# Kernel optimization log

Measured on AMD Instinct MI355X. Metric: run time of the kernel, lower is better.

## Reference

```python
import jax, jax.numpy as jnp
import numpy as np

B, S, L = 8, 64, 6          # graphs, spatial side, orientation layers
K = 6                       # Chebyshev order
IN_D, HID, OUT_D = 3, 128, 10


def _grid_edges(num_graphs, s, l):
    b, o, y, x = np.meshgrid(np.arange(num_graphs), np.arange(l), np.arange(s), np.arange(s), indexing='ij')
    nid = ((b * l + o) * s + y) * s + x  # linear node id, [B,L,s,s]
    srcs, dsts = [], []
    def add(a, c):
        srcs.append(a.ravel()); dsts.append(c.ravel())
    add(nid[..., :-1], nid[..., 1:]); add(nid[..., 1:], nid[..., :-1])                 # x-neighbors
    add(nid[:, :, :-1, :], nid[:, :, 1:, :]); add(nid[:, :, 1:, :], nid[:, :, :-1, :])  # y-neighbors
    nxt = np.roll(nid, -1, axis=1)                                                     # orientation ring
    add(nid, nxt); add(nxt, nid)
    return np.stack([np.concatenate(srcs), np.concatenate(dsts)]).astype(np.int32)


def _cluster_spatial(num_graphs, s, l):
    b, o, y, x = np.meshgrid(np.arange(num_graphs), np.arange(l), np.arange(s), np.arange(s), indexing='ij')
    h = s // 2
    return (((b * l + o) * h + y // 2) * h + x // 2).ravel().astype(np.int32)


def setup_inputs() -> dict:
    key = jax.random.key(0)
    ks = jax.random.split(key, 20)
    inp = {}
    N1 = B * L * S * S
    inp['x'] = jax.random.normal(ks[0], (N1, IN_D), jnp.float32)
    for i, s in enumerate([S, S // 2, S // 4]):
        ei = _grid_edges(B, s, L)
        inp[f'edge_index{i+1}'] = jnp.asarray(ei)
        inp[f'edge_attr{i+1}'] = jax.random.uniform(ks[1 + i], (ei.shape[1],), jnp.float32, 0.1, 1.0)
    inp['cluster1'] = jnp.asarray(_cluster_spatial(B, S, L))
    inp['cluster2'] = jnp.asarray(_cluster_spatial(B, S // 2, L))
    inp['cluster3'] = jnp.asarray(_cluster_spatial(B, S // 4, L))
    s4 = S // 8
    b, o, y, x = np.meshgrid(np.arange(B), np.arange(L), np.arange(s4), np.arange(s4), indexing='ij')
    inp['cluster4'] = jnp.asarray(((b * s4 + y) * s4 + x).ravel().astype(np.int32))  # collapse orientation axis
    inp['batch_final'] = jnp.asarray(np.repeat(np.arange(B), s4 * s4).astype(np.int32))
    dims = [(IN_D, HID), (HID, HID), (HID, HID), (HID, HID), (HID, HID), (HID, OUT_D)]
    for i, (di, do) in enumerate(dims):
        inp[f'W{i+1}'] = jax.random.normal(ks[8 + i], (K, di, do), jnp.float32) / np.float32(np.sqrt(di * K))
        inp[f'b{i+1}'] = jnp.zeros((do,), jnp.float32)
    for i in range(5):
        inp[f'gamma{i+1}'] = jnp.ones((HID,), jnp.float32)
        inp[f'beta{i+1}'] = jnp.zeros((HID,), jnp.float32)
    return inp


def _cheb_conv(x, ei, ea, W, b):
    # Chebyshev polynomial graph conv: out = sum_k T_k(L) x @ W_k + b,
    # with T0=x, T1=Lx, Tk = 2 L T_{k-1} - T_{k-2}; L applied via edge gather/scatter.
    src, dst = ei[0], ei[1]
    n = x.shape[0]
    def lap(v):
        return jax.ops.segment_sum(ea[:, None] * v[src], dst, num_segments=n)
    Tx0 = x
    out = Tx0 @ W[0]
    Tx1 = lap(x)
    out = out + Tx1 @ W[1]
    for k in range(2, W.shape[0]):
        Tx2 = 2.0 * lap(Tx1) - Tx0
        out = out + Tx2 @ W[k]
        Tx0, Tx1 = Tx1, Tx2
    return out + b


def _bn(x, g, bt):
    # BatchNorm1d in training mode (batch statistics, biased variance, eps=1e-5)
    mu = x.mean(0)
    var = x.var(0)
    return g * (x - mu) * jax.lax.rsqrt(var + 1e-5) + bt


def reference(x, edge_index1, edge_attr1, edge_index2, edge_attr2, edge_index3, edge_attr3, cluster1, cluster2, cluster3, cluster4, batch_final, W1, b1, W2, b2, W3, b3, W4, b4, W5, b5, W6, b6, gamma1, beta1, gamma2, beta2, gamma3, beta3, gamma4, beta4, gamma5, beta5):
    h = jax.nn.relu(_bn(_cheb_conv(x, edge_index1, edge_attr1, W1, b1), gamma1, beta1))
    h = jax.nn.relu(_bn(_cheb_conv(h, edge_index1, edge_attr1, W2, b2), gamma2, beta2))
    h = jax.ops.segment_max(h, cluster1, num_segments=B * L * (S // 2) ** 2)
    h = jax.nn.relu(_bn(_cheb_conv(h, edge_index2, edge_attr2, W3, b3), gamma3, beta3))
    h = jax.nn.relu(_bn(_cheb_conv(h, edge_index2, edge_attr2, W4, b4), gamma4, beta4))
    h = jax.ops.segment_max(h, cluster2, num_segments=B * L * (S // 4) ** 2)
    h = jax.nn.relu(_bn(_cheb_conv(h, edge_index3, edge_attr3, W5, b5), gamma5, beta5))
    h = jax.nn.relu(_cheb_conv(h, edge_index3, edge_attr3, W6, b6))
    h = jax.ops.segment_max(h, cluster3, num_segments=B * L * (S // 8) ** 2)   # spatial pool 3
    h = jax.ops.segment_max(h, cluster4, num_segments=B * (S // 8) ** 2)        # orientation pool
    g = jax.ops.segment_max(h, batch_final, num_segments=B)                     # global max pool
    return jax.nn.log_softmax(g, axis=1)
```

## Files before the change

kernel.cpp:

```cpp
#include <hip/hip_runtime.h>
#include <math.h>

#define L_OR 6
#define N_BL 48

typedef unsigned short u16;
typedef __attribute__((ext_vector_type(8))) short s8v;
typedef __attribute__((ext_vector_type(4))) float f4v;

#define N1 196608
#define N2 49152
#define N3 12288
#define LSTRIDE 114688

__device__ u16   g_cat[(size_t)N1 * 768 + 1024];
__device__ u16   g_O[(size_t)N1 * 128];
__device__ float g_Tt[5 * (size_t)N1 * 3];
__device__ u16   g_Bt[4 * LSTRIDE];
__device__ u16   g_W6t[16 * 768];
__device__ float g_wt1[(size_t)N1 * 8];
__device__ float g_wt2[(size_t)N2 * 8];
__device__ float g_wt3[(size_t)N3 * 8];
__device__ float g_O10[(size_t)N3 * 10];
__device__ float g_part[1536 * 256];
__device__ float g_part2[64 * 256];
__device__ float g_gsc[128];
__device__ float g_gso[128];
__device__ unsigned g_cnt;

__device__ __forceinline__ float b2f(u16 v) {
    return __uint_as_float(((unsigned)v) << 16);
}
__device__ __forceinline__ u16 f2b(float f) {
    unsigned u = __float_as_uint(f);
    return (u16)((u + 0x7FFFu + ((u >> 16) & 1u)) >> 16);
}

__global__ __launch_bounds__(256)
void eaprep_all(float* __restrict__ wt1, float* __restrict__ wt2,
                float* __restrict__ wt3, const float* __restrict__ ea1,
                const float* __restrict__ ea2, const float* __restrict__ ea3)
{
    int idx = blockIdx.x * 256 + threadIdx.x;
    int S, n; float* wtab; const float* ea;
    if (idx < N1)            { S = 64; wtab = wt1; ea = ea1; n = idx; }
    else if (idx < N1 + N2)  { S = 32; wtab = wt2; ea = ea2; n = idx - N1; }
    else if (idx < N1 + N2 + N3) { S = 16; wtab = wt3; ea = ea3; n = idx - N1 - N2; }
    else return;
    int x = n % S, y = (n / S) % S, g = n / (S * S);
    int o = g % L_OR, b = g / L_OR;
    const int szx = N_BL * S * (S - 1);
    const int basex = (g * S + y) * (S - 1);
    float wxm = (x > 0)     ? ea[basex + x - 1] : 0.f;
    float wxp = (x < S - 1) ? ea[szx + basex + x] : 0.f;
    float wym = (y > 0)     ? ea[2 * szx + (g * (S - 1) + y - 1) * S + x] : 0.f;
    float wyp = (y < S - 1) ? ea[3 * szx + (g * (S - 1) + y) * S + x] : 0.f;
    int op_ = (o == 0) ? L_OR - 1 : o - 1;
    int on_ = (o == L_OR - 1) ? 0 : o + 1;
    int sp = ((b * L_OR + op_) * S + y) * S + x;
    int sn = ((b * L_OR + on_) * S + y) * S + x;
    float wom = ea[4 * szx + sp];
    float wop = ea[4 * szx + N_BL * S * S + n];
    float* w = wtab + (size_t)n * 8;
    w[0] = wxm; w[1] = wxp; w[2] = wym; w[3] = wyp; w[4] = wom; w[5] = wop;
    ((int*)w)[6] = sp - n;
    ((int*)w)[7] = sn - n;
}

template<int S>
__global__ __launch_bounds__(256)
void lap128b(u16* __restrict__ cat, int outSlot, int inSlot, int tppSlot,
             const float* __restrict__ wtab, float alpha)
{
    const int NN = N_BL * S * S;
    int node = blockIdx.x * 16 + (threadIdx.x >> 4);
    int c8   = threadIdx.x & 15;

    float4 wa = *(const float4*)(wtab + (size_t)node * 8);
    float4 wb = *(const float4*)(wtab + (size_t)node * 8 + 4);
    int dsp = __float_as_int(wb.z);
    int dsn = __float_as_int(wb.w);
    int sxm = (node > 0)      ? node - 1 : 0;
    int sxp = (node < NN - 1) ? node + 1 : node;
    int sym = (node >= S)     ? node - S : node;
    int syp = (node < NN - S) ? node + S : node;

    const int chOff = inSlot * 128 + c8 * 8;
    float a[8] = {0.f, 0.f, 0.f, 0.f, 0.f, 0.f, 0.f, 0.f};
    auto gather = [&](int src, float w) {
        s8v v = *(const s8v*)(cat + (size_t)src * 768 + chOff);
#pragma unroll
        for (int j = 0; j < 8; ++j) a[j] += w * b2f((u16)v[j]);
    };
    gather(sxm, wa.x); gather(sxp, wa.y); gather(sym, wa.z); gather(syp, wa.w);
    gather(node + dsp, wb.x); gather(node + dsn, wb.y);

    float r[8];
#pragma unroll
    for (int j = 0; j < 8; ++j) r[j] = alpha * a[j];
    if (tppSlot >= 0) {
        s8v t = *(const s8v*)(cat + (size_t)node * 768 + tppSlot * 128 + c8 * 8);
#pragma unroll
        for (int j = 0; j < 8; ++j) r[j] -= b2f((u16)t[j]);
    }
    uint4 ov;
    asm("v_cvt_pk_bf16_f32 %0, %1, %2" : "=v"(ov.x) : "v"(r[0]), "v"(r[1]));
    asm("v_cvt_pk_bf16_f32 %0, %1, %2" : "=v"(ov.y) : "v"(r[2]), "v"(r[3]));
    asm("v_cvt_pk_bf16_f32 %0, %1, %2" : "=v"(ov.z) : "v"(r[4]), "v"(r[5]));
    asm("v_cvt_pk_bf16_f32 %0, %1, %2" : "=v"(ov.w) : "v"(r[6]), "v"(r[7]));
    *(uint4*)(cat + (size_t)node * 768 + outSlot * 128 + c8 * 8) = ov;
}

template<int S>
__global__ __launch_bounds__(256)
void lap1bn(u16* __restrict__ cat, const u16* __restrict__ O,
            int t0Slot, int t1Slot, const float* __restrict__ wtab,
            const float* __restrict__ gsc, const float* __restrict__ gso)
{
    const int NN = N_BL * S * S;
    int node = blockIdx.x * 16 + (threadIdx.x >> 4);
    int c8   = threadIdx.x & 15;

    float4 wa = *(const float4*)(wtab + (size_t)node * 8);
    float4 wb = *(const float4*)(wtab + (size_t)node * 8 + 4);
    int dsp = __float_as_int(wb.z);
    int dsn = __float_as_int(wb.w);
    int sxm = (node > 0)      ? node - 1 : 0;
    int sxp = (node < NN - 1) ? node + 1 : node;
    int sym = (node >= S)     ? node - S : node;
    int syp = (node < NN - S) ? node + S : node;

    float sc[8], so[8];
    {
        float4 s0 = *(const float4*)(gsc + c8 * 8);
        float4 s1 = *(const float4*)(gsc + c8 * 8 + 4);
        float4 o0 = *(const float4*)(gso + c8 * 8);
        float4 o1 = *(const float4*)(gso + c8 * 8 + 4);
        sc[0]=s0.x; sc[1]=s0.y; sc[2]=s0.z; sc[3]=s0.w;
        sc[4]=s1.x; sc[5]=s1.y; sc[6]=s1.z; sc[7]=s1.w;
        so[0]=o0.x; so[1]=o0.y; so[2]=o0.z; so[3]=o0.w;
        so[4]=o1.x; so[5]=o1.y; so[6]=o1.z; so[7]=o1.w;
    }

    float a[8] = {0.f, 0.f, 0.f, 0.f, 0.f, 0.f, 0.f, 0.f};
    auto gatherbn = [&](int src, float w) {
        s8v v = *(const s8v*)(O + (size_t)src * 128 + c8 * 8);
#pragma unroll
        for (int j = 0; j < 8; ++j)
            a[j] += w * fmaxf(b2f((u16)v[j]) * sc[j] + so[j], 0.f);
    };
    gatherbn(sxm, wa.x); gatherbn(sxp, wa.y); gatherbn(sym, wa.z); gatherbn(syp, wa.w);
    gatherbn(node + dsp, wb.x); gatherbn(node + dsn, wb.y);

    float t0[8];
    {
        s8v v = *(const s8v*)(O + (size_t)node * 128 + c8 * 8);
#pragma unroll
        for (int j = 0; j < 8; ++j)
            t0[j] = fmaxf(b2f((u16)v[j]) * sc[j] + so[j], 0.f);
    }
    uint4 o0v, o1v;
    asm("v_cvt_pk_bf16_f32 %0, %1, %2" : "=v"(o0v.x) : "v"(t0[0]), "v"(t0[1]));
    asm("v_cvt_pk_bf16_f32 %0, %1, %2" : "=v"(o0v.y) : "v"(t0[2]), "v"(t0[3]));
    asm("v_cvt_pk_bf16_f32 %0, %1, %2" : "=v"(o0v.z) : "v"(t0[4]), "v"(t0[5]));
    asm("v_cvt_pk_bf16_f32 %0, %1, %2" : "=v"(o0v.w) : "v"(t0[6]), "v"(t0[7]));
    asm("v_cvt_pk_bf16_f32 %0, %1, %2" : "=v"(o1v.x) : "v"(a[0]), "v"(a[1]));
    asm("v_cvt_pk_bf16_f32 %0, %1, %2" : "=v"(o1v.y) : "v"(a[2]), "v"(a[3]));
    asm("v_cvt_pk_bf16_f32 %0, %1, %2" : "=v"(o1v.z) : "v"(a[4]), "v"(a[5]));
    asm("v_cvt_pk_bf16_f32 %0, %1, %2" : "=v"(o1v.w) : "v"(a[6]), "v"(a[7]));
    *(uint4*)(cat + (size_t)node * 768 + t0Slot * 128 + c8 * 8) = o0v;
    *(uint4*)(cat + (size_t)node * 768 + t1Slot * 128 + c8 * 8) = o1v;
}

template<int S>
__global__ __launch_bounds__(256)
void lap3_kernel(float* __restrict__ out, const float* __restrict__ in,
                 const float* __restrict__ tpp, const float* __restrict__ wtab,
                 float alpha)
{
    const int NN = N_BL * S * S;
    int n = blockIdx.x * 256 + threadIdx.x;
    if (n >= NN) return;
    float4 wa = *(const float4*)(wtab + (size_t)n * 8);
    float4 wb = *(const float4*)(wtab + (size_t)n * 8 + 4);
    int dsp = __float_as_int(wb.z);
    int dsn = __float_as_int(wb.w);
    int sxm = (n > 0)      ? n - 1 : 0;
    int sxp = (n < NN - 1) ? n + 1 : n;
    int sym = (n >= S)     ? n - S : n;
    int syp = (n < NN - S) ? n + S : n;

    float a0 = 0.f, a1 = 0.f, a2 = 0.f;
    auto gather = [&](int src, float w) {
        a0 += w * in[src * 3 + 0];
        a1 += w * in[src * 3 + 1];
        a2 += w * in[src * 3 + 2];
    };
    gather(sxm, wa.x); gather(sxp, wa.y); gather(sym, wa.z); gather(syp, wa.w);
    gather(n + dsp, wb.x); gather(n + dsn, wb.y);

    float r0 = alpha * a0, r1 = alpha * a1, r2 = alpha * a2;
    if (tpp) { r0 -= tpp[n * 3 + 0]; r1 -= tpp[n * 3 + 1]; r2 -= tpp[n * 3 + 2]; }
    out[n * 3 + 0] = r0; out[n * 3 + 1] = r1; out[n * 3 + 2] = r2;
}

__global__ __launch_bounds__(256)
void gemm_mfma_cat(u16* __restrict__ O, const u16* __restrict__ A,
                   const u16* __restrict__ Bf, const float* __restrict__ bias,
                   float* __restrict__ partials)
{
    __shared__ u16 Bs[4][4096];
    const int tid  = threadIdx.x;
    const int wave = tid >> 6;
    const int lane = tid & 63;
    const int lrow = lane & 15;
    const int kg   = lane >> 4;
    const int r0   = blockIdx.x * 128 + wave * 32;

    const u16* A0 = A + (size_t)(r0 + lrow) * 768 + kg * 8;
    const u16* A1 = A0 + (size_t)16 * 768;

    f4v acc[2][8] = {};

#pragma unroll
    for (int i = 0; i < 4; ++i) {
        *(s8v*)&Bs[i][tid * 8]        = *(const s8v*)(Bf + i * 4096 + tid * 8);
        *(s8v*)&Bs[i][2048 + tid * 8] = *(const s8v*)(Bf + i * 4096 + 2048 + tid * 8);
    }
    s8v a0 = *(const s8v*)(A0);
    s8v a1 = *(const s8v*)(A1);
    __syncthreads();

#pragma unroll 1
    for (int p = 0; p < 24; ++p) {
        const int pl = (p + 4 < 24) ? p + 4 : 23;
        s8v nb0 = *(const s8v*)(Bf + pl * 4096 + tid * 8);
        s8v nb1 = *(const s8v*)(Bf + pl * 4096 + 2048 + tid * 8);
        s8v na0 = *(const s8v*)(A0 + (p + 1) * 32);
        s8v na1 = *(const s8v*)(A1 + (p + 1) * 32);
        const u16* bsl = &Bs[p & 3][0];
#pragma unroll
        for (int ct = 0; ct < 8; ++ct) {
            s8v b = *(const s8v*)&bsl[(ct * 64 + lane) * 8];
            acc[0][ct] = __builtin_amdgcn_mfma_f32_16x16x32_bf16(a0, b, acc[0][ct], 0, 0, 0);
            acc[1][ct] = __builtin_amdgcn_mfma_f32_16x16x32_bf16(a1, b, acc[1][ct], 0, 0, 0);
        }
        __syncthreads();
        *(s8v*)&Bs[p & 3][tid * 8]        = nb0;
        *(s8v*)&Bs[p & 3][2048 + tid * 8] = nb1;
        a0 = na0; a1 = na1;
    }

    __shared__ float sred[4][2][8][16];
    float cs[8], cq[8];
#pragma unroll
    for (int ct = 0; ct < 8; ++ct) { cs[ct] = 0.f; cq[ct] = 0.f; }

#pragma unroll
    for (int s = 0; s < 2; ++s)
#pragma unroll
        for (int ct = 0; ct < 8; ++ct) {
            int col = ct * 16 + lrow;
            float bv = bias[col];
#pragma unroll
            for (int j = 0; j < 4; ++j) {
                int row = r0 + s * 16 + kg * 4 + j;
                float v = acc[s][ct][j] + bv;
                O[(size_t)row * 128 + col] = f2b(v);
                cs[ct] += v; cq[ct] += v * v;
            }
        }
#pragma unroll
    for (int ct = 0; ct < 8; ++ct) {
        cs[ct] += __shfl_xor(cs[ct], 16); cs[ct] += __shfl_xor(cs[ct], 32);
        cq[ct] += __shfl_xor(cq[ct], 16); cq[ct] += __shfl_xor(cq[ct], 32);
    }
    __syncthreads();
    if (lane < 16) {
#pragma unroll
        for (int ct = 0; ct < 8; ++ct) {
            sred[wave][0][ct][lane] = cs[ct];
            sred[wave][1][ct][lane] = cq[ct];
        }
    }
    __syncthreads();
    if (threadIdx.x < 128) {
        int ct = threadIdx.x >> 4, lr = threadIdx.x & 15;
        float S = 0.f, Q = 0.f;
#pragma unroll
        for (int w = 0; w < 4; ++w) { S += sred[w][0][ct][lr]; Q += sred[w][1][ct][lr]; }
        partials[blockIdx.x * 256 + threadIdx.x]       = S;
        partials[blockIdx.x * 256 + 128 + threadIdx.x] = Q;
    }
}

__global__ __launch_bounds__(256)
void wprep_all(const float* __restrict__ W2, const float* __restrict__ W3,
               const float* __restrict__ W4, const float* __restrict__ W5,
               u16* __restrict__ Bf)
{
    int l = blockIdx.y;
    const float* W = (l == 0) ? W2 : (l == 1) ? W3 : (l == 2) ? W4 : W5;
    int base = (l & 1) ? 5 : 0;
    int idx = blockIdx.x * 256 + threadIdx.x;
    int j    = idx & 7;
    int lane = (idx >> 3) & 63;
    int ct   = (idx >> 9) & 7;
    int k0s  = idx >> 12;
    int k    = k0s * 32 + (lane >> 4) * 8 + j;
    int col  = ct * 16 + (lane & 15);
    int slot = k >> 7, d = k & 127;
    int wk = slot - base; if (wk < 0) wk += 6;
    Bf[(size_t)l * LSTRIDE + idx] = f2b(W[(size_t)wk * 16384 + d * 128 + col]);
}

__global__ __launch_bounds__(256)
void w6prep(const float* __restrict__ W, u16* __restrict__ W6t, int base)
{
    int idx = blockIdx.x * 256 + threadIdx.x;
    if (idx >= 16 * 768) return;
    int c = idx / 768, kk = idx % 768;
    int slot = kk >> 7, d = kk & 127;
    int wk = slot - base; if (wk < 0) wk += 6;
    W6t[idx] = (c < 10) ? f2b(W[(size_t)wk * 1280 + d * 10 + c]) : (u16)0;
}

__global__ __launch_bounds__(256)
void l1gemm(u16* __restrict__ O, const float* __restrict__ T0,
            const float* __restrict__ Tt, const float* __restrict__ W,
            const float* __restrict__ bias, float* __restrict__ partials)
{
    __shared__ float Ts[128][18];
    __shared__ float sh[2][128], sh2[2][128];
    int tid = threadIdx.x;
    int rbase = blockIdx.x * 128;
    for (int i = tid; i < 128 * 18; i += 256) {
        int r = i / 18, t = i % 18;
        int k = t / 3, j = t % 3;
        Ts[r][t] = (k == 0) ? T0[(size_t)(rbase + r) * 3 + j]
                            : Tt[(size_t)(k - 1) * N1 * 3 + (size_t)(rbase + r) * 3 + j];
    }
    __syncthreads();
    int c = tid & 127, h = tid >> 7;
    float w[18];
#pragma unroll
    for (int k = 0; k < 6; ++k)
#pragma unroll
        for (int j = 0; j < 3; ++j) w[k * 3 + j] = W[(size_t)k * 384 + j * 128 + c];
    float bv = bias[c];
    float S = 0.f, Q = 0.f;
    for (int i = 0; i < 64; ++i) {
        int r = h * 64 + i;
        float acc = bv;
#pragma unroll
        for (int t = 0; t < 18; ++t) acc += Ts[r][t] * w[t];
        O[(size_t)(rbase + r) * 128 + c] = f2b(acc);
        S += acc; Q += acc * acc;
    }
    sh[h][c] = S; sh2[h][c] = Q;
    __syncthreads();
    if (tid < 128) {
        partials[blockIdx.x * 256 + tid]       = sh[0][tid] + sh[1][tid];
        partials[blockIdx.x * 256 + 128 + tid] = sh2[0][tid] + sh2[1][tid];
    }
}

__global__ __launch_bounds__(256)
void out10_cat(float* __restrict__ O10, const u16* __restrict__ cat,
               const u16* __restrict__ W6t, const float* __restrict__ bias)
{
    int col = threadIdx.x & 15;
    int row = blockIdx.x * 16 + (threadIdx.x >> 4);
    const u16* a = cat + (size_t)row * 768;
    const u16* w = W6t + (size_t)col * 768;
    float acc = 0.f;
#pragma unroll 4
    for (int k0 = 0; k0 < 768; k0 += 8) {
        s8v av = *(const s8v*)(a + k0);
        s8v wv = *(const s8v*)(w + k0);
#pragma unroll
        for (int j = 0; j < 8; ++j)
            acc += b2f((u16)av[j]) * b2f((u16)wv[j]);
    }
    if (col < 10)
        O10[(size_t)row * 10 + col] = fmaxf(acc + bias[col], 0.f);
}

__global__ __launch_bounds__(256)
void bn_reduce_f(const float* __restrict__ partials, int nblk, int N,
                 const float* __restrict__ g, const float* __restrict__ bt,
                 float* __restrict__ gsc, float* __restrict__ gso,
                 float* __restrict__ part2, unsigned* __restrict__ cnt)
{
    int tid = threadIdx.x;
    float S = 0.f;
#pragma unroll 4
    for (int b = blockIdx.x; b < nblk; b += 64)
        S += partials[(size_t)b * 256 + tid];
    part2[blockIdx.x * 256 + tid] = S;
    __threadfence();
    __syncthreads();
    __shared__ int last;
    if (tid == 0) last = (atomicAdd(cnt, 1u) == 63u) ? 1 : 0;
    __syncthreads();
    if (!last) return;
    __threadfence();
    int c = tid & 127, h = tid >> 7;
    float Sa = 0.f, Qa = 0.f;
#pragma unroll 8
    for (int b = h; b < 64; b += 2) {
        Sa += part2[b * 256 + c];
        Qa += part2[b * 256 + 128 + c];
    }
    __shared__ float shS[2][128], shQ[2][128];
    shS[h][c] = Sa; shQ[h][c] = Qa;
    __syncthreads();
    if (tid < 128) {
        float Sx = shS[0][tid] + shS[1][tid];
        float Qx = shQ[0][tid] + shQ[1][tid];
        float inv_n = 1.f / (float)N;
        float mu = Sx * inv_n;
        float var = Qx * inv_n - mu * mu;
        float is = rsqrtf(var + 1e-5f);
        float sc = is * g[tid];
        gsc[tid] = sc;
        gso[tid] = bt[tid] - mu * sc;
    }
    if (tid == 0) *cnt = 0u;
}

__global__ __launch_bounds__(256)
void bn_apply_pool8(const u16* __restrict__ O, u16* __restrict__ cat, int outSlot,
                    int s, int Nout,
                    const float* __restrict__ gsc, const float* __restrict__ gso)
{
    int idx = blockIdx.x * 256 + threadIdx.x;
    if (idx >= Nout * 16) return;
    int c8 = idx & 15;
    int n2 = idx >> 4;
    int h  = s >> 1;
    int x2 = n2 % h;
    int y2 = (n2 / h) % h;
    int gg = n2 / (h * h);
    int base = (gg * s + 2 * y2) * s + 2 * x2;
    s8v v0 = *(const s8v*)(O + (size_t)base * 128 + c8 * 8);
    s8v v1 = *(const s8v*)(O + (size_t)(base + 1) * 128 + c8 * 8);
    s8v v2 = *(const s8v*)(O + (size_t)(base + s) * 128 + c8 * 8);
    s8v v3 = *(const s8v*)(O + (size_t)(base + s + 1) * 128 + c8 * 8);
    s8v ov;
#pragma unroll
    for (int j = 0; j < 8; ++j) {
        int c = c8 * 8 + j;
        float sc = gsc[c], so = gso[c];
        float m =          b2f((u16)v0[j]) * sc + so;
        m = fmaxf(m, b2f((u16)v1[j]) * sc + so);
        m = fmaxf(m, b2f((u16)v2[j]) * sc + so);
        m = fmaxf(m, b2f((u16)v3[j]) * sc + so);
        ov[j] = (short)f2b(fmaxf(m, 0.f));
    }
    *(s8v*)(cat + (size_t)n2 * 768 + outSlot * 128 + c8 * 8) = ov;
}

__global__ __launch_bounds__(512)
void tail_fused(const float* __restrict__ O10, float* __restrict__ out)
{
    __shared__ float p4[512][10];
    __shared__ float G[8][10];
    __shared__ float rowm[8], rowl[8];
    int t = threadIdx.x;
    for (int i = t; i < 5120; i += 512) {
        int c = i % 10, n = i / 10;
        int x = n & 7, y = (n >> 3) & 7, b = n >> 6;
        float m = -INFINITY;
        for (int o = 0; o < L_OR; ++o) {
            int base = ((b * L_OR + o) * 16 + 2 * y) * 16 + 2 * x;
            m = fmaxf(m, O10[(size_t)base * 10 + c]);
            m = fmaxf(m, O10[(size_t)(base + 1) * 10 + c]);
            m = fmaxf(m, O10[(size_t)(base + 16) * 10 + c]);
            m = fmaxf(m, O10[(size_t)(base + 17) * 10 + c]);
        }
        p4[n][c] = m;
    }
    __syncthreads();
    if (t < 80) {
        int b = t / 10, c = t % 10;
        float m = -INFINITY;
        for (int p = 0; p < 64; ++p) m = fmaxf(m, p4[b * 64 + p][c]);
        G[b][c] = m;
    }
    __syncthreads();
    if (t < 8) {
        float m = -INFINITY;
        for (int c = 0; c < 10; ++c) m = fmaxf(m, G[t][c]);
        float s = 0.f;
        for (int c = 0; c < 10; ++c) s += expf(G[t][c] - m);
        rowm[t] = m; rowl[t] = logf(s);
    }
    __syncthreads();
    if (t < 80) {
        int b = t / 10, c = t % 10;
        out[t] = G[b][c] - rowm[b] - rowl[b];
    }
}

static void launch_lapb(u16* cat, int os, int is, int ts, const float* wtab,
                        int S, int N, float alpha, hipStream_t st)
{
    dim3 grid(N / 16), block(256);
    if (S == 64)      hipLaunchKernelGGL(lap128b<64>, grid, block, 0, st, cat, os, is, ts, wtab, alpha);
    else if (S == 32) hipLaunchKernelGGL(lap128b<32>, grid, block, 0, st, cat, os, is, ts, wtab, alpha);
    else              hipLaunchKernelGGL(lap128b<16>, grid, block, 0, st, cat, os, is, ts, wtab, alpha);
}

static void cheb_laps_b5(u16* cat, const float* wtab, int S, int N, hipStream_t st)
{
    for (int k = 1; k < 6; ++k) {
        int os = (k + 5) % 6;
        int is = (k - 1 + 5) % 6;
        int ts = (k >= 2) ? (k - 2 + 5) % 6 : -1;
        launch_lapb(cat, os, is, ts, wtab, S, N, (k == 1) ? 1.f : 2.f, st);
    }
}

static void cheb_laps_2to5(u16* cat, const float* wtab, int S, int N, hipStream_t st)
{
    for (int k = 2; k < 6; ++k)
        launch_lapb(cat, k, k - 1, k - 2, wtab, S, N, 2.f, st);
}

static void launch_lap1bn(u16* cat, const u16* O, const float* wtab,
                          const float* gsc, const float* gso,
                          int S, int N, hipStream_t st)
{
    dim3 grid(N / 16), block(256);
    if (S == 64)      hipLaunchKernelGGL(lap1bn<64>, grid, block, 0, st, cat, O, 0, 1, wtab, gsc, gso);
    else if (S == 32) hipLaunchKernelGGL(lap1bn<32>, grid, block, 0, st, cat, O, 0, 1, wtab, gsc, gso);
    else              hipLaunchKernelGGL(lap1bn<16>, grid, block, 0, st, cat, O, 0, 1, wtab, gsc, gso);
}

extern "C" void kernel_launch(void* const* d_in, const int* in_sizes, int n_in,
                              void* d_out, int out_size, void* d_ws, size_t ws_size,
                              hipStream_t stream)
{
    const float* x   = (const float*)d_in[0];
    const float* ea1 = (const float*)d_in[2];
    const float* ea2 = (const float*)d_in[4];
    const float* ea3 = (const float*)d_in[6];
    const float* W1  = (const float*)d_in[12];
    const float* b1  = (const float*)d_in[13];
    const float* W2  = (const float*)d_in[14];
    const float* b2  = (const float*)d_in[15];
    const float* W3  = (const float*)d_in[16];
    const float* b3  = (const float*)d_in[17];
    const float* W4  = (const float*)d_in[18];
    const float* b4  = (const float*)d_in[19];
    const float* W5  = (const float*)d_in[20];
    const float* b5  = (const float*)d_in[21];
    const float* W6  = (const float*)d_in[22];
    const float* b6  = (const float*)d_in[23];
    const float* g1  = (const float*)d_in[24];
    const float* be1 = (const float*)d_in[25];
    const float* g2  = (const float*)d_in[26];
    const float* be2 = (const float*)d_in[27];
    const float* g3  = (const float*)d_in[28];
    const float* be3 = (const float*)d_in[29];
    const float* g4  = (const float*)d_in[30];
    const float* be4 = (const float*)d_in[31];
    const float* g5  = (const float*)d_in[32];
    const float* be5 = (const float*)d_in[33];

    u16 *cat, *O, *Bt, *W6t;
    float *Tt, *O10, *part, *part2, *gsc, *gso, *wt1, *wt2, *wt3;
    unsigned* cnt;
    if (hipGetSymbolAddress((void**)&cat, HIP_SYMBOL(g_cat)) != hipSuccess) return;
    if (hipGetSymbolAddress((void**)&O,   HIP_SYMBOL(g_O))   != hipSuccess) return;
    if (hipGetSymbolAddress((void**)&Tt,  HIP_SYMBOL(g_Tt))  != hipSuccess) return;
    if (hipGetSymbolAddress((void**)&Bt,  HIP_SYMBOL(g_Bt))  != hipSuccess) return;
    if (hipGetSymbolAddress((void**)&W6t, HIP_SYMBOL(g_W6t)) != hipSuccess) return;
    if (hipGetSymbolAddress((void**)&O10, HIP_SYMBOL(g_O10)) != hipSuccess) return;
    if (hipGetSymbolAddress((void**)&part,  HIP_SYMBOL(g_part))  != hipSuccess) return;
    if (hipGetSymbolAddress((void**)&part2, HIP_SYMBOL(g_part2)) != hipSuccess) return;
    if (hipGetSymbolAddress((void**)&gsc, HIP_SYMBOL(g_gsc)) != hipSuccess) return;
    if (hipGetSymbolAddress((void**)&gso, HIP_SYMBOL(g_gso)) != hipSuccess) return;
    if (hipGetSymbolAddress((void**)&wt1, HIP_SYMBOL(g_wt1)) != hipSuccess) return;
    if (hipGetSymbolAddress((void**)&wt2, HIP_SYMBOL(g_wt2)) != hipSuccess) return;
    if (hipGetSymbolAddress((void**)&wt3, HIP_SYMBOL(g_wt3)) != hipSuccess) return;
    if (hipGetSymbolAddress((void**)&cnt, HIP_SYMBOL(g_cnt)) != hipSuccess) return;

    dim3 blk(256);

    hipLaunchKernelGGL(eaprep_all, dim3((N1 + N2 + N3) / 256), blk, 0, stream,
                       wt1, wt2, wt3, ea1, ea2, ea3);
    hipLaunchKernelGGL(wprep_all, dim3(384, 4), blk, 0, stream, W2, W3, W4, W5, Bt);
    hipLaunchKernelGGL(w6prep, dim3(48), blk, 0, stream, W6, W6t, 0);

    {
        float* t1 = Tt;
        float* t2 = Tt + (size_t)N1 * 3;
        float* t3 = Tt + (size_t)2 * N1 * 3;
        float* t4 = Tt + (size_t)3 * N1 * 3;
        float* t5 = Tt + (size_t)4 * N1 * 3;
        dim3 gl((N1 + 255) / 256);
        hipLaunchKernelGGL(lap3_kernel<64>, gl, blk, 0, stream, t1, x,  (const float*)nullptr, wt1, 1.f);
        hipLaunchKernelGGL(lap3_kernel<64>, gl, blk, 0, stream, t2, t1, x,  wt1, 2.f);
        hipLaunchKernelGGL(lap3_kernel<64>, gl, blk, 0, stream, t3, t2, t1, wt1, 2.f);
        hipLaunchKernelGGL(lap3_kernel<64>, gl, blk, 0, stream, t4, t3, t2, wt1, 2.f);
        hipLaunchKernelGGL(lap3_kernel<64>, gl, blk, 0, stream, t5, t4, t3, wt1, 2.f);
        hipLaunchKernelGGL(l1gemm, dim3(N1 / 128), blk, 0, stream, O, x, Tt, W1, b1, part);
    }
    hipLaunchKernelGGL(bn_reduce_f, dim3(64), blk, 0, stream, part, N1 / 128, N1,
                       g1, be1, gsc, gso, part2, cnt);

    launch_lap1bn(cat, O, wt1, gsc, gso, 64, N1, stream);
    cheb_laps_2to5(cat, wt1, 64, N1, stream);
    hipLaunchKernelGGL(gemm_mfma_cat, dim3(N1 / 128), blk, 0, stream, O, cat, Bt, b2, part);
    hipLaunchKernelGGL(bn_reduce_f, dim3(64), blk, 0, stream, part, N1 / 128, N1,
                       g2, be2, gsc, gso, part2, cnt);
    hipLaunchKernelGGL(bn_apply_pool8, dim3(N2 / 16), blk, 0, stream,
                       O, cat, 5, 64, N2, gsc, gso);

    cheb_laps_b5(cat, wt2, 32, N2, stream);
    hipLaunchKernelGGL(gemm_mfma_cat, dim3(N2 / 128), blk, 0, stream, O, cat, Bt + 1 * LSTRIDE, b3, part);
    hipLaunchKernelGGL(bn_reduce_f, dim3(64), blk, 0, stream, part, N2 / 128, N2,
                       g3, be3, gsc, gso, part2, cnt);

    launch_lap1bn(cat, O, wt2, gsc, gso, 32, N2, stream);
    cheb_laps_2to5(cat, wt2, 32, N2, stream);
    hipLaunchKernelGGL(gemm_mfma_cat, dim3(N2 / 128), blk, 0, stream, O, cat, Bt + 2 * LSTRIDE, b4, part);
    hipLaunchKernelGGL(bn_reduce_f, dim3(64), blk, 0, stream, part, N2 / 128, N2,
                       g4, be4, gsc, gso, part2, cnt);
    hipLaunchKernelGGL(bn_apply_pool8, dim3(N3 / 16), blk, 0, stream,
                       O, cat, 5, 32, N3, gsc, gso);

    cheb_laps_b5(cat, wt3, 16, N3, stream);
    hipLaunchKernelGGL(gemm_mfma_cat, dim3(N3 / 128), blk, 0, stream, O, cat, Bt + 3 * LSTRIDE, b5, part);
    hipLaunchKernelGGL(bn_reduce_f, dim3(64), blk, 0, stream, part, N3 / 128, N3,
                       g5, be5, gsc, gso, part2, cnt);

    launch_lap1bn(cat, O, wt3, gsc, gso, 16, N3, stream);
    cheb_laps_2to5(cat, wt3, 16, N3, stream);
    hipLaunchKernelGGL(out10_cat, dim3(N3 / 16), blk, 0, stream, O10, cat, W6t, b6);

    hipLaunchKernelGGL(tail_fused, dim3(1), dim3(512), 0, stream, O10, (float*)d_out);
}
```

Before: 787.7 us.

## Stage GEMM weights via direct global-to-LDS loads with double buffering

The MFMA GEMM now copies each weight tile straight from global memory into LDS with global_load_lds, instead of loading into registers and then storing to shared memory. It double-buffers 64-wide K chunks (12 iterations instead of 24), which halves the number of barriers and drops one redundant sync in the epilogue. The W6 prep kernel is folded into wprep_all as a fifth grid row, saving a launch. The risk is the prefetch distance: it shrinks from four chunks to one, so global latency may be less well hidden.

```diff
diff --git a/kernel.cpp b/kernel.cpp
--- a/kernel.cpp
+++ b/kernel.cpp
@@ -209,7 +209,7 @@
                    const u16* __restrict__ Bf, const float* __restrict__ bias,
                    float* __restrict__ partials)
 {
-    __shared__ u16 Bs[4][4096];
+    __shared__ u16 Bs[2][8192];
     const int tid  = threadIdx.x;
     const int wave = tid >> 6;
     const int lane = tid & 63;
@@ -222,33 +222,46 @@
 
     f4v acc[2][8] = {};
 
-#pragma unroll
-    for (int i = 0; i < 4; ++i) {
-        *(s8v*)&Bs[i][tid * 8]        = *(const s8v*)(Bf + i * 4096 + tid * 8);
-        *(s8v*)&Bs[i][2048 + tid * 8] = *(const s8v*)(Bf + i * 4096 + 2048 + tid * 8);
-    }
-    s8v a0 = *(const s8v*)(A0);
-    s8v a1 = *(const s8v*)(A1);
+    auto stage = [&](int q, int slot) {
+        const char* src = (const char*)(Bf + q * 8192) + wave * 4096 + lane * 16;
+        char* dstb = (char*)(&Bs[slot][0]) + wave * 4096;
+#pragma unroll
+        for (int i = 0; i < 4; ++i)
+            __builtin_amdgcn_global_load_lds(
+                (const __attribute__((address_space(1))) unsigned*)(src + i * 1024),
+                (__attribute__((address_space(3))) unsigned*)(dstb + i * 1024),
+                16, 0, 0);
+    };
+
+    stage(0, 0);
+    s8v a00 = *(const s8v*)(A0);
+    s8v a10 = *(const s8v*)(A1);
+    s8v a01 = *(const s8v*)(A0 + 32);
+    s8v a11 = *(const s8v*)(A1 + 32);
     __syncthreads();
 
 #pragma unroll 1
-    for (int p = 0; p < 24; ++p) {
-        const int pl = (p + 4 < 24) ? p + 4 : 23;
-        s8v nb0 = *(const s8v*)(Bf + pl * 4096 + tid * 8);
-        s8v nb1 = *(const s8v*)(Bf + pl * 4096 + 2048 + tid * 8);
-        s8v na0 = *(const s8v*)(A0 + (p + 1) * 32);
-        s8v na1 = *(const s8v*)(A1 + (p + 1) * 32);
-        const u16* bsl = &Bs[p & 3][0];
+    for (int p = 0; p < 12; ++p) {
+        stage(p + 1, (p + 1) & 1);
+        s8v na00 = *(const s8v*)(A0 + (p + 1) * 64);
+        s8v na10 = *(const s8v*)(A1 + (p + 1) * 64);
+        s8v na01 = *(const s8v*)(A0 + (p + 1) * 64 + 32);
+        s8v na11 = *(const s8v*)(A1 + (p + 1) * 64 + 32);
+        const u16* bsl = &Bs[p & 1][0];
 #pragma unroll
         for (int ct = 0; ct < 8; ++ct) {
             s8v b = *(const s8v*)&bsl[(ct * 64 + lane) * 8];
-            acc[0][ct] = __builtin_amdgcn_mfma_f32_16x16x32_bf16(a0, b, acc[0][ct], 0, 0, 0);
-            acc[1][ct] = __builtin_amdgcn_mfma_f32_16x16x32_bf16(a1, b, acc[1][ct], 0, 0, 0);
+            acc[0][ct] = __builtin_amdgcn_mfma_f32_16x16x32_bf16(a00, b, acc[0][ct], 0, 0, 0);
+            acc[1][ct] = __builtin_amdgcn_mfma_f32_16x16x32_bf16(a10, b, acc[1][ct], 0, 0, 0);
+        }
+#pragma unroll
+        for (int ct = 0; ct < 8; ++ct) {
+            s8v b = *(const s8v*)&bsl[4096 + (ct * 64 + lane) * 8];
+            acc[0][ct] = __builtin_amdgcn_mfma_f32_16x16x32_bf16(a01, b, acc[0][ct], 0, 0, 0);
+            acc[1][ct] = __builtin_amdgcn_mfma_f32_16x16x32_bf16(a11, b, acc[1][ct], 0, 0, 0);
         }
         __syncthreads();
-        *(s8v*)&Bs[p & 3][tid * 8]        = nb0;
-        *(s8v*)&Bs[p & 3][2048 + tid * 8] = nb1;
-        a0 = na0; a1 = na1;
+        a00 = na00; a10 = na10; a01 = na01; a11 = na11;
     }
 
     __shared__ float sred[4][2][8][16];
@@ -275,7 +288,6 @@
         cs[ct] += __shfl_xor(cs[ct], 16); cs[ct] += __shfl_xor(cs[ct], 32);
         cq[ct] += __shfl_xor(cq[ct], 16); cq[ct] += __shfl_xor(cq[ct], 32);
     }
-    __syncthreads();
     if (lane < 16) {
 #pragma unroll
         for (int ct = 0; ct < 8; ++ct) {
@@ -297,12 +309,20 @@
 __global__ __launch_bounds__(256)
 void wprep_all(const float* __restrict__ W2, const float* __restrict__ W3,
                const float* __restrict__ W4, const float* __restrict__ W5,
-               u16* __restrict__ Bf)
+               const float* __restrict__ W6, u16* __restrict__ Bf,
+               u16* __restrict__ W6t)
 {
     int l = blockIdx.y;
+    int idx = blockIdx.x * 256 + threadIdx.x;
+    if (l == 4) {
+        if (idx >= 16 * 768) return;
+        int c = idx / 768, kk = idx % 768;
+        int slot = kk >> 7, d = kk & 127;
+        W6t[idx] = (c < 10) ? f2b(W6[(size_t)slot * 1280 + d * 10 + c]) : (u16)0;
+        return;
+    }
     const float* W = (l == 0) ? W2 : (l == 1) ? W3 : (l == 2) ? W4 : W5;
     int base = (l & 1) ? 5 : 0;
-    int idx = blockIdx.x * 256 + threadIdx.x;
     int j    = idx & 7;
     int lane = (idx >> 3) & 63;
     int ct   = (idx >> 9) & 7;
@@ -312,17 +332,6 @@
     int slot = k >> 7, d = k & 127;
     int wk = slot - base; if (wk < 0) wk += 6;
     Bf[(size_t)l * LSTRIDE + idx] = f2b(W[(size_t)wk * 16384 + d * 128 + col]);
-}
-
-__global__ __launch_bounds__(256)
-void w6prep(const float* __restrict__ W, u16* __restrict__ W6t, int base)
-{
-    int idx = blockIdx.x * 256 + threadIdx.x;
-    if (idx >= 16 * 768) return;
-    int c = idx / 768, kk = idx % 768;
-    int slot = kk >> 7, d = kk & 127;
-    int wk = slot - base; if (wk < 0) wk += 6;
-    W6t[idx] = (c < 10) ? f2b(W[(size_t)wk * 1280 + d * 10 + c]) : (u16)0;
 }
 
 __global__ __launch_bounds__(256)
@@ -591,8 +600,7 @@
 
     hipLaunchKernelGGL(eaprep_all, dim3((N1 + N2 + N3) / 256), blk, 0, stream,
                        wt1, wt2, wt3, ea1, ea2, ea3);
-    hipLaunchKernelGGL(wprep_all, dim3(384, 4), blk, 0, stream, W2, W3, W4, W5, Bt);
-    hipLaunchKernelGGL(w6prep, dim3(48), blk, 0, stream, W6, W6t, 0);
+    hipLaunchKernelGGL(wprep_all, dim3(384, 5), blk, 0, stream, W2, W3, W4, W5, W6, Bt, W6t);
 
     {
         float* t1 = Tt;
```

After: 795.1 us. About the same (+0.9%).
